# Performance work log

Hardware: AMD Instinct MI355X
Metric: run time of the kernel (lower is better)

## Reference

```python
import jax, jax.numpy as jnp
import numpy as np

N = 50000      # nodes
E = 200000     # edges
F_IN = 128     # input features
H = 1024       # hidden
C = 16         # classes
K = 3          # TAGConv hops
EPS = 1e-5


def setup_inputs() -> dict:
    key = jax.random.key(0)
    ks = jax.random.split(key, 12)
    s = 0.02
    x = jax.random.normal(ks[0], (N, F_IN), jnp.float32)
    edge_index = jax.random.randint(ks[1], (2, E), 0, N, dtype=jnp.int64)
    weight = jax.random.uniform(ks[2], (E,), jnp.float32)
    return {
        "x": x,
        "edge_index": edge_index,
        "weight": weight,
        "W1": jax.random.normal(ks[3], (K + 1, F_IN, H), jnp.float32) * s,
        "b1": jnp.zeros((H,), jnp.float32),
        "g1": jnp.ones((H,), jnp.float32),
        "be1": jnp.zeros((H,), jnp.float32),
        "a1": jnp.ones((H,), jnp.float32),
        "W2": jax.random.normal(ks[4], (K + 1, H, H), jnp.float32) * s,
        "b2": jnp.zeros((H,), jnp.float32),
        "g2": jnp.ones((H,), jnp.float32),
        "be2": jnp.zeros((H,), jnp.float32),
        "a2": jnp.ones((H,), jnp.float32),
        "W3": jax.random.normal(ks[5], (K + 1, H, C), jnp.float32) * s,
        "b3": jnp.zeros((C,), jnp.float32),
    }


def _edge_norm(weight, src, dst):
    # gcn_norm without self-loops: deg from edge weights at target nodes
    deg = jax.ops.segment_sum(weight, dst, num_segments=N)
    safe = jnp.where(deg > 0, deg, 1.0)
    dinv = jnp.where(deg > 0, jax.lax.rsqrt(safe), 0.0)
    norm_w = dinv[src] * weight * dinv[dst]
    cnt = jax.ops.segment_sum(jnp.ones((E,), weight.dtype), dst, num_segments=N)
    cnt_inv = jnp.where(cnt > 0, 1.0 / jnp.where(cnt > 0, cnt, 1.0), 0.0)
    return norm_w, cnt_inv


def _tagconv(x, W, b, src, dst, norm_w, cnt_inv):
    # out = sum_k lin_k(x_k), x_k = mean-aggr of norm_w * x_{k-1}[src] at dst
    out = x @ W[0]
    h = x
    for k in range(1, K + 1):
        msg = norm_w[:, None] * h[src]                       # [E, d]
        h = jax.ops.segment_sum(msg, dst, num_segments=N) * cnt_inv[:, None]
        out = out + h @ W[k]
    return out + b


def _graphnorm(x, g, be, a):
    # single graph: per-graph stats = global stats over nodes
    mean = jnp.mean(x, axis=0)
    out = x - a * mean
    var = jnp.mean(out * out, axis=0)
    return g * out / jnp.sqrt(var + EPS) + be


def reference(x, edge_index, weight, W1, b1, g1, be1, a1,
              W2, b2, g2, be2, a2, W3, b3):
    src, dst = edge_index[0], edge_index[1]
    norm_w, cnt_inv = _edge_norm(weight, src, dst)
    h = jax.nn.elu(_tagconv(x, W1, b1, src, dst, norm_w, cnt_inv))
    h = _graphnorm(h, g1, be1, a1)
    h = jax.nn.elu(_tagconv(h, W2, b2, src, dst, norm_w, cnt_inv))
    h = _graphnorm(h, g2, be2, a2)
    return _tagconv(h, W3, b3, src, dst, norm_w, cnt_inv)
```

## Files before the change

### kernel.cpp

```cpp
#include <hip/hip_runtime.h>
#include <hip/hip_bf16.h>
#include <math.h>

#define N_NODES 50000
#define N_EDGES 200000
#define FIN 128
#define HID 1024
#define NCLS 16
#define EPSN 1e-5f
#define NPAD 50048
#define MT 391
#define EPITCH 136

typedef __attribute__((ext_vector_type(8))) short short8;
typedef __attribute__((ext_vector_type(8))) unsigned short ushort8;
typedef __attribute__((ext_vector_type(4))) unsigned short u16x4;
typedef __attribute__((ext_vector_type(4))) float f32x4;

static __device__ __forceinline__ float bf2f(unsigned short u) {
  union { unsigned int i; float f; } v; v.i = ((unsigned int)u) << 16; return v.f;
}
static __device__ __forceinline__ unsigned short f2bf(float f) {
  __hip_bfloat16 h = __float2bfloat16(f);
  return *(unsigned short*)&h;
}

#define ASYNC16(gsrc, ldst)                                                   \
  __builtin_amdgcn_global_load_lds(                                           \
      (const __attribute__((address_space(1))) void*)(gsrc),                  \
      (__attribute__((address_space(3))) void*)(ldst), 16, 0, 0)


__global__ __launch_bounds__(256) void k_deg_cnt(const int* __restrict__ dst,
                                                 const float* __restrict__ w,
                                                 float* deg, int* cnt) {
  int e = blockIdx.x * 256 + threadIdx.x;
  if (e < N_EDGES) {
    int d = dst[e];
    atomicAdd(&deg[d], w[e]);
    atomicAdd(&cnt[d], 1);
  }
}

__global__ __launch_bounds__(256) void k_normw(const int* __restrict__ src,
                                               const int* __restrict__ dst,
                                               const float* __restrict__ w,
                                               const float* __restrict__ deg,
                                               float* __restrict__ normw) {
  int e = blockIdx.x * 256 + threadIdx.x;
  if (e < N_EDGES) {
    float ds = deg[src[e]], dd = deg[dst[e]];
    float a = ds > 0.f ? rsqrtf(ds) : 0.f;
    float b = dd > 0.f ? rsqrtf(dd) : 0.f;
    normw[e] = a * w[e] * b;
  }
}

__global__ __launch_bounds__(256) void k_cntinv(const int* __restrict__ cnt,
                                                float* __restrict__ cnt_inv) {
  int n = blockIdx.x * 256 + threadIdx.x;
  if (n < N_NODES) {
    int c = cnt[n];
    cnt_inv[n] = c > 0 ? 1.f / (float)c : 0.f;
  }
}

__global__ __launch_bounds__(1024) void k_scan_a(const int* __restrict__ cnt,
                                                 int* __restrict__ rowptr,
                                                 int* __restrict__ bsums) {
  __shared__ int sm[1024];
  int tid = threadIdx.x;
  int i = blockIdx.x * 1024 + tid;
  int v = (i < N_NODES) ? cnt[i] : 0;
  sm[tid] = v;
  __syncthreads();
  for (int off = 1; off < 1024; off <<= 1) {
    int t = (tid >= off) ? sm[tid - off] : 0;
    __syncthreads();
    sm[tid] += t;
    __syncthreads();
  }
  if (i < N_NODES) rowptr[i] = sm[tid] - v;
  if (tid == 1023) bsums[blockIdx.x] = sm[1023];
}

__global__ void k_scan_b(int* bsums, int nb) {
  if (threadIdx.x == 0 && blockIdx.x == 0) {
    int s = 0;
    for (int i = 0; i < nb; ++i) { int t = bsums[i]; bsums[i] = s; s += t; }
  }
}

__global__ __launch_bounds__(1024) void k_scan_c(int* __restrict__ rowptr,
                                                 const int* __restrict__ bsums) {
  int i = blockIdx.x * 1024 + threadIdx.x;
  if (i < N_NODES) rowptr[i] += bsums[blockIdx.x];
}

__global__ __launch_bounds__(256) void k_fill(const int* __restrict__ src,
                                              const int* __restrict__ dst,
                                              const float* __restrict__ normw,
                                              const int* __restrict__ rowptr,
                                              int* __restrict__ fill,
                                              int2* __restrict__ csr_ew) {
  int e = blockIdx.x * 256 + threadIdx.x;
  if (e < N_EDGES) {
    int d = dst[e];
    int pos = rowptr[d] + atomicAdd(&fill[d], 1);
    csr_ew[pos] = make_int2(src[e], __float_as_int(normw[e]));
  }
}


__global__ void k_transpose_bf16(const float* __restrict__ in,
                                 __hip_bfloat16* __restrict__ out, int K, int N) {
  __shared__ float tile[32][33];
  int kb = blockIdx.x * 32, nb = blockIdx.y * 32;
  int tx = threadIdx.x, ty = threadIdx.y;
  for (int i = ty; i < 32; i += 8) tile[i][tx] = in[(size_t)(kb + i) * N + nb + tx];
  __syncthreads();
  for (int i = ty; i < 32; i += 8)
    out[(size_t)(nb + i) * K + kb + tx] = __float2bfloat16(tile[tx][i]);
}

__global__ void k_transpose_scale_bf16(const float* __restrict__ in,
                                       __hip_bfloat16* __restrict__ out, int K, int N,
                                       const float* __restrict__ alpha) {
  __shared__ float tile[32][33];
  int kb = blockIdx.x * 32, nb = blockIdx.y * 32;
  int tx = threadIdx.x, ty = threadIdx.y;
  for (int i = ty; i < 32; i += 8) tile[i][tx] = in[(size_t)(kb + i) * N + nb + tx];
  __syncthreads();
  float sc = alpha[(kb + tx) & (HID - 1)];
  for (int i = ty; i < 32; i += 8)
    out[(size_t)(nb + i) * K + kb + tx] = __float2bfloat16(tile[tx][i] * sc);
}

__global__ __launch_bounds__(256) void k_ck(const float* __restrict__ W2,
                                            const float* __restrict__ beta,
                                            const float* __restrict__ b2,
                                            float* __restrict__ ck) {
  int k3 = blockIdx.x, tid = threadIdx.x;
  float acc[4] = {0.f, 0.f, 0.f, 0.f};
  const float* Wk = W2 + (size_t)k3 * HID * HID;
  for (int in = 0; in < HID; ++in) {
    float s = beta[in];
    const float* row = Wk + (size_t)in * HID;
#pragma unroll
    for (int j = 0; j < 4; ++j) acc[j] += s * row[tid + j * 256];
  }
#pragma unroll
  for (int j = 0; j < 4; ++j) {
    float v = acc[j];
    if (k3 == 0) v += b2[tid + j * 256];
    ck[k3 * HID + tid + j * 256] = v;
  }
}

__global__ __launch_bounds__(256) void k_packw3(const float* __restrict__ W3,
                                                __hip_bfloat16* __restrict__ W3T) {
  int idx = blockIdx.x * 256 + threadIdx.x;
  if (idx < 4 * 1024 * 16) {
    int k3 = idx >> 14, r = idx & 16383, k = r >> 4, j = r & 15;
    W3T[(size_t)(k3 * 16 + j) * 1024 + k] = __float2bfloat16(W3[idx]);
  }
}

__global__ __launch_bounds__(256) void k_x_to_bf16(const float* __restrict__ x,
                                                   unsigned short* __restrict__ xc) {
  int i = blockIdx.x * 256 + threadIdx.x;
  if (i < N_NODES * FIN / 4) {
    int n = i >> 5, c4 = i & 31;
    const float4 v = ((const float4*)x)[i];
    u16x4 o;
    o[0] = f2bf(v.x); o[1] = f2bf(v.y); o[2] = f2bf(v.z); o[3] = f2bf(v.w);
    *(u16x4*)&xc[(size_t)n * 512 + c4 * 4] = o;
  }
}


template <int W>
__global__ __launch_bounds__(256) void k_spmm_v(
    const unsigned short* __restrict__ src_t, int sp,
    unsigned short* __restrict__ dst_t, int dp,
    const int* __restrict__ rowptr, const int* __restrict__ cnt,
    const float* __restrict__ cnt_inv,
    const int2* __restrict__ csr_ew) {
  constexpr int G = W / 8;
  int gl = blockIdx.x * 256 + threadIdx.x;
  int node = gl / G;
  if (node >= N_NODES) return;
  int fl = (gl % G) * 8;
  int beg = rowptr[node], ne = cnt[node];
  float acc[8] = {0.f, 0.f, 0.f, 0.f, 0.f, 0.f, 0.f, 0.f};
  for (int i = 0; i < ne; ++i) {
    int2 e = csr_ew[beg + i];
    float wt = __int_as_float(e.y);
    ushort8 v = *(const ushort8*)&src_t[(size_t)e.x * sp + fl];
#pragma unroll
    for (int j = 0; j < 8; ++j) acc[j] += wt * bf2f(v[j]);
  }
  float ci = cnt_inv[node];
  ushort8 o;
#pragma unroll
  for (int j = 0; j < 8; ++j) o[j] = f2bf(acc[j] * ci);
  *(ushort8*)&dst_t[(size_t)node * dp + fl] = o;
}

__global__ __launch_bounds__(256) void k_spmm16(const float* __restrict__ src_t, int sp,
                                                const float* __restrict__ addend, int ap,
                                                const float* __restrict__ b3,
                                                float* __restrict__ out, int op,
                                                const int* __restrict__ rowptr,
                                                const int* __restrict__ cnt,
                                                const float* __restrict__ cnt_inv,
                                                const int2* __restrict__ csr_ew) {
  int idx = blockIdx.x * 256 + threadIdx.x;
  if (idx >= N_NODES * 16) return;
  int node = idx >> 4, f = idx & 15;
  int beg = rowptr[node], ne = cnt[node];
  float acc = 0.f;
  for (int i = 0; i < ne; ++i) {
    int2 e = csr_ew[beg + i];
    acc += __int_as_float(e.y) * src_t[(size_t)e.x * sp + f];
  }
  float r = acc * cnt_inv[node] + addend[(size_t)node * ap + f];
  if (b3) r += b3[f];
  out[(size_t)node * op + f] = r;
}


__global__ __launch_bounds__(256, 4) void k_gemm(
    const unsigned short* __restrict__ A, int lda,
    const unsigned short* __restrict__ BT, int ldb,
    const unsigned short* __restrict__ Cinit, int ldci,
    void* __restrict__ Cout, int ldc, int cbf16,
    int M, int Nout, int K,
    const float* __restrict__ bias, int do_elu) {
  __shared__ __align__(16) unsigned short smem[128 * EPITCH];
  int tid = threadIdx.x;
  int wave = tid >> 6, lane = tid & 63;
  int wm = wave >> 1, wn = wave & 1;
  int l15 = lane & 15, quad = lane >> 4;
  int im = blockIdx.y, in_ = blockIdx.x;

  f32x4 acc[4][4];
  if (Cinit) {
    {
      int r = tid >> 1, hf = tid & 1;
      const unsigned short* gsrc =
          &Cinit[(size_t)(im * 128 + r) * ldci + in_ * 128 + hf * 64];
#pragma unroll
      for (int v = 0; v < 8; ++v)
        *(ushort8*)&smem[r * EPITCH + hf * 64 + v * 8] = *(const ushort8*)&gsrc[v * 8];
    }
    __syncthreads();
#pragma unroll
    for (int i = 0; i < 4; ++i)
#pragma unroll
      for (int j = 0; j < 4; ++j)
#pragma unroll
        for (int reg = 0; reg < 4; ++reg)
          acc[i][j][reg] =
              bf2f(smem[(wm * 64 + i * 16 + quad * 4 + reg) * EPITCH + wn * 64 + j * 16 + l15]);
    __syncthreads();
  } else {
#pragma unroll
    for (int i = 0; i < 4; ++i)
#pragma unroll
      for (int j = 0; j < 4; ++j) acc[i][j] = (f32x4){0.f, 0.f, 0.f, 0.f};
  }

  int srow = tid >> 2;
  int sl = (tid & 3) ^ (srow & 3) ^ ((srow >> 2) & 3);
  const unsigned short* gA0 = &A[(size_t)(im * 128 + srow) * lda + sl * 8];
  const unsigned short* gA1 = &A[(size_t)(im * 128 + 64 + srow) * lda + sl * 8];
  const unsigned short* gB0 = &BT[(size_t)(in_ * 128 + srow) * ldb + sl * 8];
  const unsigned short* gB1 = &BT[(size_t)(in_ * 128 + 64 + srow) * ldb + sl * 8];
  unsigned short* ldsA = smem;
  unsigned short* ldsB = smem + 8192;
  int woff0 = (wave * 64) * 8;
  int woff1 = (256 + wave * 64) * 8;
  int rsl = (quad ^ (l15 & 3) ^ (l15 >> 2)) * 8;

  auto stage = [&](int k0, int p) {
    ASYNC16(gA0 + k0, &ldsA[p * 4096 + woff0]);
    ASYNC16(gA1 + k0, &ldsA[p * 4096 + woff1]);
    ASYNC16(gB0 + k0, &ldsB[p * 4096 + woff0]);
    ASYNC16(gB1 + k0, &ldsB[p * 4096 + woff1]);
  };
  auto compute = [&](int p) {
    short8 af[4], bf[4];
#pragma unroll
    for (int i = 0; i < 4; ++i)
      af[i] = *(const short8*)&ldsA[p * 4096 + (wm * 64 + i * 16 + l15) * 32 + rsl];
#pragma unroll
    for (int j = 0; j < 4; ++j)
      bf[j] = *(const short8*)&ldsB[p * 4096 + (wn * 64 + j * 16 + l15) * 32 + rsl];
#pragma unroll
    for (int i = 0; i < 4; ++i)
#pragma unroll
      for (int j = 0; j < 4; ++j)
        acc[i][j] = __builtin_amdgcn_mfma_f32_16x16x32_bf16(af[i], bf[j], acc[i][j], 0, 0, 0);
  };

  stage(0, 0);
  __syncthreads();
  int p = 0;
  for (int k0 = 32; k0 < K; k0 += 32) {
    stage(k0, p ^ 1);
    compute(p);
    __syncthreads();
    p ^= 1;
  }
  compute(p);
  __syncthreads();

  if (cbf16) {
#pragma unroll
    for (int i = 0; i < 4; ++i)
#pragma unroll
      for (int j = 0; j < 4; ++j) {
        int cg = in_ * 128 + wn * 64 + j * 16 + l15;
        float bv = bias ? bias[cg] : 0.f;
#pragma unroll
        for (int reg = 0; reg < 4; ++reg) {
          float v = acc[i][j][reg] + bv;
          if (do_elu) v = v > 0.f ? v : expm1f(v);
          smem[(wm * 64 + i * 16 + quad * 4 + reg) * EPITCH + wn * 64 + j * 16 + l15] = f2bf(v);
        }
      }
    __syncthreads();
    int r = tid >> 1, hf = tid & 1;
    unsigned short* gdst =
        (unsigned short*)Cout + (size_t)(im * 128 + r) * ldc + in_ * 128 + hf * 64;
#pragma unroll
    for (int v = 0; v < 8; ++v)
      *(ushort8*)&gdst[v * 8] = *(const ushort8*)&smem[r * EPITCH + hf * 64 + v * 8];
  } else {
#pragma unroll
    for (int i = 0; i < 4; ++i) {
      int r0 = im * 128 + wm * 64 + i * 16 + quad * 4;
#pragma unroll
      for (int j = 0; j < 4; ++j) {
        int c = in_ * 128 + wn * 64 + j * 16 + l15;
        if (c < Nout) {
#pragma unroll
          for (int reg = 0; reg < 4; ++reg) {
            int r = r0 + reg;
            if (r < M) {
              float v = acc[i][j][reg];
              if (bias) v += bias[c];
              if (do_elu) v = v > 0.f ? v : expm1f(v);
              ((float*)Cout)[(size_t)r * ldc + c] = v;
            }
          }
        }
      }
    }
  }
}


__global__ __launch_bounds__(512) void k_colstats(const unsigned short* __restrict__ h,
                                                  float* __restrict__ stats) {
  __shared__ float sm[4 * 2048];
  int tid = threadIdx.x;
  int f0 = (tid & 127) * 8;
  int q = tid >> 7;
  int r0 = blockIdx.y * 128 + q * 32;
  int r1 = r0 + 32; if (r1 > N_NODES) r1 = N_NODES;
  float s[8] = {0,0,0,0,0,0,0,0}, s2[8] = {0,0,0,0,0,0,0,0};
  for (int r = r0; r < r1; ++r) {
    ushort8 v = *(const ushort8*)&h[(size_t)r * HID + f0];
#pragma unroll
    for (int j = 0; j < 8; ++j) { float x = bf2f(v[j]); s[j] += x; s2[j] += x * x; }
  }
#pragma unroll
  for (int j = 0; j < 8; ++j) {
    sm[q * 2048 + f0 + j] = s[j];
    sm[q * 2048 + 1024 + f0 + j] = s2[j];
  }
  __syncthreads();
  for (int idx = tid; idx < 2048; idx += 512) {
    float v = sm[idx] + sm[2048 + idx] + sm[4096 + idx] + sm[6144 + idx];
    atomicAdd(&stats[idx], v);
  }
}

__global__ __launch_bounds__(256) void k_finalize(const float* __restrict__ g,
                                                  const float* __restrict__ be,
                                                  const float* __restrict__ a,
                                                  float* __restrict__ stats) {
  int f = blockIdx.x * 256 + threadIdx.x;
  if (f < HID) {
    float m = stats[f] / (float)N_NODES;
    float ex2 = stats[HID + f] / (float)N_NODES;
    float av = a[f];
    float var = ex2 - 2.f * av * m * m + av * av * m * m;
    float alpha = g[f] * rsqrtf(var + EPSN);
    stats[2 * HID + f] = alpha;
    stats[3 * HID + f] = be[f] - alpha * av * m;
  }
}

__global__ __launch_bounds__(256) void k_normalize(unsigned short* __restrict__ h,
                                                   const float* __restrict__ stats) {
  int i = blockIdx.x * 256 + threadIdx.x;
  if (i < N_NODES * HID / 8) {
    int f0 = (i * 8) & 1023;
    ushort8 v = *(ushort8*)&h[(size_t)i * 8];
#pragma unroll
    for (int j = 0; j < 8; ++j)
      v[j] = f2bf(stats[2 * HID + f0 + j] * bf2f(v[j]) + stats[3 * HID + f0 + j]);
    *(ushort8*)&h[(size_t)i * 8] = v;
  }
}


extern "C" void kernel_launch(void* const* d_in, const int* in_sizes, int n_in,
                              void* d_out, int out_size, void* d_ws, size_t ws_size,
                              hipStream_t stream) {
  const float* x   = (const float*)d_in[0];
  const int*   ei  = (const int*)d_in[1];
  const float* w   = (const float*)d_in[2];
  const float* W1  = (const float*)d_in[3];
  const float* b1  = (const float*)d_in[4];
  const float* g1  = (const float*)d_in[5];
  const float* be1 = (const float*)d_in[6];
  const float* a1  = (const float*)d_in[7];
  const float* W2  = (const float*)d_in[8];
  const float* b2  = (const float*)d_in[9];
  const float* g2  = (const float*)d_in[10];
  const float* be2 = (const float*)d_in[11];
  const float* a2  = (const float*)d_in[12];
  const float* W3  = (const float*)d_in[13];
  const float* b3  = (const float*)d_in[14];
  float* out = (float*)d_out;

  const int* srcI = ei;
  const int* dstI = ei + N_EDGES;

  char* base = (char*)d_ws;
  size_t off = 0;
  auto alloc = [&](size_t bytes) -> char* {
    char* p = base + off;
    off += (bytes + 255) & ~(size_t)255;
    return p;
  };

  float* deg      = (float*)alloc(N_NODES * 4);
  int*   cnt      = (int*)alloc(N_NODES * 4);
  float* cnt_inv  = (float*)alloc(N_NODES * 4);
  float* normw    = (float*)alloc(N_EDGES * 4);
  int*   rowptr   = (int*)alloc((N_NODES + 1) * 4);
  int*   fill     = (int*)alloc(N_NODES * 4);
  int*   bsums    = (int*)alloc(64 * 4);
  int2*  csr_ew   = (int2*)alloc((size_t)N_EDGES * 8);
  float* stats    = (float*)alloc(4 * HID * 4);
  float* ck       = (float*)alloc(4 * HID * 4);
  __hip_bfloat16* W1T = (__hip_bfloat16*)alloc((size_t)1024 * 512 * 2);
  __hip_bfloat16* W2T = (__hip_bfloat16*)alloc((size_t)1024 * 4096 * 2);
  __hip_bfloat16* W3T = (__hip_bfloat16*)alloc((size_t)128 * 1024 * 2);
  const size_t FT = (size_t)NPAD * HID * 2;
  unsigned short* T0 = (unsigned short*)alloc(FT);
  unsigned short* T1 = (unsigned short*)alloc(FT);
  size_t rem = (ws_size > off) ? (ws_size - off) : 0;
  bool full = rem >= FT + 1024;
  unsigned short *T2 = nullptr, *Q = nullptr, *R = nullptr;
  int wcols = 0;
  if (full) {
    T2 = (unsigned short*)alloc(FT);
  } else {
    wcols = 512;
    if (rem < 2 * (size_t)NPAD * 512 * 2 + 1024) wcols = 256;
    if (wcols == 256 && rem < 2 * (size_t)NPAD * 256 * 2 + 1024) wcols = 128;
    Q = (unsigned short*)alloc((size_t)NPAD * wcols * 2);
    R = (unsigned short*)alloc((size_t)NPAD * wcols * 2);
  }
  float* Z  = (float*)T0;
  float* t0 = (float*)((char*)T0 + (size_t)16 * 1024 * 1024);
  float* t1 = (float*)((char*)T0 + (size_t)24 * 1024 * 1024);
  (void)n_in; (void)in_sizes; (void)out_size;

  const int EB = (N_EDGES + 255) / 256;
  const int NB = (N_NODES + 255) / 256;

  (void)hipMemsetAsync(deg, 0, N_NODES * 4, stream);
  (void)hipMemsetAsync(cnt, 0, N_NODES * 4, stream);
  (void)hipMemsetAsync(fill, 0, N_NODES * 4, stream);
  k_deg_cnt<<<EB, 256, 0, stream>>>(dstI, w, deg, cnt);
  k_normw<<<EB, 256, 0, stream>>>(srcI, dstI, w, deg, normw);
  k_cntinv<<<NB, 256, 0, stream>>>(cnt, cnt_inv);
  k_scan_a<<<49, 1024, 0, stream>>>(cnt, rowptr, bsums);
  k_scan_b<<<1, 64, 0, stream>>>(bsums, 49);
  k_scan_c<<<49, 1024, 0, stream>>>(rowptr, bsums);
  k_fill<<<EB, 256, 0, stream>>>(srcI, dstI, normw, rowptr, fill, csr_ew);

  k_transpose_bf16<<<dim3(512 / 32, 1024 / 32), dim3(32, 8), 0, stream>>>(W1, W1T, 512, 1024);
  k_packw3<<<(65536 + 255) / 256, 256, 0, stream>>>(W3, W3T);

  const unsigned short* W2Tu = (const unsigned short*)W2T;

  k_x_to_bf16<<<(N_NODES * FIN / 4 + 255) / 256, 256, 0, stream>>>(x, T1);
  {
    int blocks = (N_NODES * 16 + 255) / 256;
    for (int k = 1; k <= 3; ++k)
      k_spmm_v<128><<<blocks, 256, 0, stream>>>(
          T1 + (k - 1) * FIN, 512, T1 + k * FIN, 512,
          rowptr, cnt, cnt_inv, csr_ew);
  }
  k_gemm<<<dim3(8, MT), 256, 0, stream>>>(
      T1, 512, (const unsigned short*)W1T, 512,
      nullptr, 0, T0, HID, 1, N_NODES, HID, 512, b1, 1);
  (void)hipMemsetAsync(stats, 0, 2 * HID * 4, stream);
  k_colstats<<<dim3(1, MT), 512, 0, stream>>>(T0, stats);
  k_finalize<<<4, 256, 0, stream>>>(g1, be1, a1, stats);
  k_transpose_scale_bf16<<<dim3(4096 / 32, 1024 / 32), dim3(32, 8), 0, stream>>>(
      W2, W2T, 4096, 1024, stats + 2 * HID);
  k_ck<<<4, 256, 0, stream>>>(W2, stats + 3 * HID, b2, ck);

  if (full) {
    const int SPB = (N_NODES * 128 + 255) / 256;
    k_gemm<<<dim3(8, MT), 256, 0, stream>>>(
        T0, 1024, W2Tu + 3 * 1024, 4096,
        nullptr, 0, T1, 1024, 1, N_NODES, 1024, 1024, ck + 3 * 1024, 0);
    k_spmm_v<1024><<<SPB, 256, 0, stream>>>(T1, 1024, T2, 1024,
                                            rowptr, cnt, cnt_inv, csr_ew);
    k_gemm<<<dim3(8, MT), 256, 0, stream>>>(
        T0, 1024, W2Tu + 2 * 1024, 4096,
        T2, 1024, T1, 1024, 1, N_NODES, 1024, 1024, ck + 2 * 1024, 0);
    k_spmm_v<1024><<<SPB, 256, 0, stream>>>(T1, 1024, T2, 1024,
                                            rowptr, cnt, cnt_inv, csr_ew);
    k_gemm<<<dim3(8, MT), 256, 0, stream>>>(
        T0, 1024, W2Tu + 1 * 1024, 4096,
        T2, 1024, T1, 1024, 1, N_NODES, 1024, 1024, ck + 1 * 1024, 0);
    k_spmm_v<1024><<<SPB, 256, 0, stream>>>(T1, 1024, T2, 1024,
                                            rowptr, cnt, cnt_inv, csr_ew);
    k_gemm<<<dim3(8, MT), 256, 0, stream>>>(
        T0, 1024, W2Tu + 0 * 1024, 4096,
        T2, 1024, T1, 1024, 1, N_NODES, 1024, 1024, ck + 0 * 1024, 1);
  } else {
    auto spmm_w = [&](const unsigned short* s, unsigned short* d) {
      int blocks = (N_NODES * (wcols / 8) + 255) / 256;
      if (wcols == 512)
        k_spmm_v<512><<<blocks, 256, 0, stream>>>(s, wcols, d, wcols,
            rowptr, cnt, cnt_inv, csr_ew);
      else if (wcols == 256)
        k_spmm_v<256><<<blocks, 256, 0, stream>>>(s, wcols, d, wcols,
            rowptr, cnt, cnt_inv, csr_ew);
      else
        k_spmm_v<128><<<blocks, 256, 0, stream>>>(s, wcols, d, wcols,
            rowptr, cnt, cnt_inv, csr_ew);
    };
    for (int c = 0; c < HID; c += wcols) {
      const unsigned short* Wb = W2Tu + (size_t)c * 4096;
      k_gemm<<<dim3(wcols / 128, MT), 256, 0, stream>>>(
          T0, 1024, Wb + 3 * 1024, 4096,
          nullptr, 0, Q, wcols, 1, N_NODES, wcols, 1024, ck + 3 * 1024 + c, 0);
      spmm_w(Q, R);
      k_gemm<<<dim3(wcols / 128, MT), 256, 0, stream>>>(
          T0, 1024, Wb + 2 * 1024, 4096,
          R, wcols, Q, wcols, 1, N_NODES, wcols, 1024, ck + 2 * 1024 + c, 0);
      spmm_w(Q, R);
      k_gemm<<<dim3(wcols / 128, MT), 256, 0, stream>>>(
          T0, 1024, Wb + 1 * 1024, 4096,
          R, wcols, Q, wcols, 1, N_NODES, wcols, 1024, ck + 1 * 1024 + c, 0);
      spmm_w(Q, R);
      k_gemm<<<dim3(wcols / 128, MT), 256, 0, stream>>>(
          T0, 1024, Wb + 0 * 1024, 4096,
          R, wcols, T1 + c, 1024, 1, N_NODES, wcols, 1024, ck + 0 * 1024 + c, 1);
    }
  }
  (void)hipMemsetAsync(stats, 0, 2 * HID * 4, stream);
  k_colstats<<<dim3(1, MT), 512, 0, stream>>>(T1, stats);
  k_finalize<<<4, 256, 0, stream>>>(g2, be2, a2, stats);
  k_normalize<<<(N_NODES * HID / 8) / 256, 256, 0, stream>>>(T1, stats);

  k_gemm<<<dim3(1, MT), 256, 0, stream>>>(
      T1, 1024, (const unsigned short*)W3T, 1024,
      nullptr, 0, Z, 64, 0, N_NODES, 64, 1024, nullptr, 0);
  const int SB = (N_NODES * 16 + 255) / 256;
  k_spmm16<<<SB, 256, 0, stream>>>(Z + 48, 64, Z + 32, 64, nullptr, t0, 16,
                                   rowptr, cnt, cnt_inv, csr_ew);
  k_spmm16<<<SB, 256, 0, stream>>>(t0, 16, Z + 16, 64, nullptr, t1, 16,
                                   rowptr, cnt, cnt_inv, csr_ew);
  k_spmm16<<<SB, 256, 0, stream>>>(t1, 16, Z + 0, 64, b3, out, 16,
                                   rowptr, cnt, cnt_inv, csr_ew);
}
```

Before: 1.978 ms.

## Fuse graphnorm column stats into GEMM epilogue and fold second norm into W3

Column sum and sum-of-squares are now accumulated in the bf16 GEMM epilogue from shared memory with atomics, which removes the separate colstats passes over the 50000x1024 activations. The second graphnorm's per-column affine is folded into W3 (scaled by alpha) and a bias term ck3, so the full normalize pass over T1 is gone. The LDS pitch changes to 132 with 8-byte accesses to cut bank conflicts, and the SpMM gather loop is unrolled by two edges. The cost is a serial per-column loop over 128 rows inside each GEMM block plus global atomics, and stats are taken from bf16-rounded outputs.

```diff
diff --git a/kernel.cpp b/kernel.cpp
--- a/kernel.cpp
+++ b/kernel.cpp
@@ -10,7 +10,7 @@
 #define EPSN 1e-5f
 #define NPAD 50048
 #define MT 391
-#define EPITCH 136
+#define EPITCH 132
 
 typedef __attribute__((ext_vector_type(8))) short short8;
 typedef __attribute__((ext_vector_type(8))) unsigned short ushort8;
@@ -157,12 +157,24 @@
   }
 }
 
+__global__ __launch_bounds__(64) void k_ck3(const float* __restrict__ W3,
+                                            const float* __restrict__ beta,
+                                            float* __restrict__ ck3) {
+  int t = threadIdx.x;
+  int k = t >> 4, j = t & 15;
+  float acc = 0.f;
+  for (int in = 0; in < HID; ++in)
+    acc += beta[in] * W3[((size_t)k * HID + in) * 16 + j];
+  ck3[t] = acc;
+}
+
 __global__ __launch_bounds__(256) void k_packw3(const float* __restrict__ W3,
-                                                __hip_bfloat16* __restrict__ W3T) {
+                                                __hip_bfloat16* __restrict__ W3T,
+                                                const float* __restrict__ alpha) {
   int idx = blockIdx.x * 256 + threadIdx.x;
   if (idx < 4 * 1024 * 16) {
     int k3 = idx >> 14, r = idx & 16383, k = r >> 4, j = r & 15;
-    W3T[(size_t)(k3 * 16 + j) * 1024 + k] = __float2bfloat16(W3[idx]);
+    W3T[(size_t)(k3 * 16 + j) * 1024 + k] = __float2bfloat16(W3[idx] * alpha[k]);
   }
 }
 
@@ -191,14 +203,23 @@
   int node = gl / G;
   if (node >= N_NODES) return;
   int fl = (gl % G) * 8;
-  int beg = rowptr[node], ne = cnt[node];
+  int beg = rowptr[node], end = beg + cnt[node];
   float acc[8] = {0.f, 0.f, 0.f, 0.f, 0.f, 0.f, 0.f, 0.f};
-  for (int i = 0; i < ne; ++i) {
-    int2 e = csr_ew[beg + i];
-    float wt = __int_as_float(e.y);
-    ushort8 v = *(const ushort8*)&src_t[(size_t)e.x * sp + fl];
-#pragma unroll
-    for (int j = 0; j < 8; ++j) acc[j] += wt * bf2f(v[j]);
+  int i = beg;
+  for (; i + 1 < end; i += 2) {
+    int2 e0 = csr_ew[i], e1 = csr_ew[i + 1];
+    float w0 = __int_as_float(e0.y), w1 = __int_as_float(e1.y);
+    ushort8 v0 = *(const ushort8*)&src_t[(size_t)e0.x * sp + fl];
+    ushort8 v1 = *(const ushort8*)&src_t[(size_t)e1.x * sp + fl];
+#pragma unroll
+    for (int j = 0; j < 8; ++j) acc[j] += w0 * bf2f(v0[j]) + w1 * bf2f(v1[j]);
+  }
+  if (i < end) {
+    int2 e0 = csr_ew[i];
+    float w0 = __int_as_float(e0.y);
+    ushort8 v0 = *(const ushort8*)&src_t[(size_t)e0.x * sp + fl];
+#pragma unroll
+    for (int j = 0; j < 8; ++j) acc[j] += w0 * bf2f(v0[j]);
   }
   float ci = cnt_inv[node];
   ushort8 o;
@@ -236,7 +257,8 @@
     const unsigned short* __restrict__ Cinit, int ldci,
     void* __restrict__ Cout, int ldc, int cbf16,
     int M, int Nout, int K,
-    const float* __restrict__ bias, int do_elu) {
+    const float* __restrict__ bias, int do_elu,
+    float* __restrict__ stats_out, int stats_off) {
   __shared__ __align__(16) unsigned short smem[128 * EPITCH];
   int tid = threadIdx.x;
   int wave = tid >> 6, lane = tid & 63;
@@ -251,8 +273,14 @@
       const unsigned short* gsrc =
           &Cinit[(size_t)(im * 128 + r) * ldci + in_ * 128 + hf * 64];
 #pragma unroll
-      for (int v = 0; v < 8; ++v)
-        *(ushort8*)&smem[r * EPITCH + hf * 64 + v * 8] = *(const ushort8*)&gsrc[v * 8];
+      for (int v = 0; v < 8; ++v) {
+        ushort8 t8 = *(const ushort8*)&gsrc[v * 8];
+        u16x4 lo, hi;
+        lo[0] = t8[0]; lo[1] = t8[1]; lo[2] = t8[2]; lo[3] = t8[3];
+        hi[0] = t8[4]; hi[1] = t8[5]; hi[2] = t8[6]; hi[3] = t8[7];
+        *(u16x4*)&smem[r * EPITCH + hf * 64 + v * 8] = lo;
+        *(u16x4*)&smem[r * EPITCH + hf * 64 + v * 8 + 4] = hi;
+      }
     }
     __syncthreads();
 #pragma unroll
@@ -335,8 +363,24 @@
     unsigned short* gdst =
         (unsigned short*)Cout + (size_t)(im * 128 + r) * ldc + in_ * 128 + hf * 64;
 #pragma unroll
-    for (int v = 0; v < 8; ++v)
-      *(ushort8*)&gdst[v * 8] = *(const ushort8*)&smem[r * EPITCH + hf * 64 + v * 8];
+    for (int v = 0; v < 8; ++v) {
+      u16x4 lo = *(const u16x4*)&smem[r * EPITCH + hf * 64 + v * 8];
+      u16x4 hi = *(const u16x4*)&smem[r * EPITCH + hf * 64 + v * 8 + 4];
+      ushort8 o;
+      o[0] = lo[0]; o[1] = lo[1]; o[2] = lo[2]; o[3] = lo[3];
+      o[4] = hi[0]; o[5] = hi[1]; o[6] = hi[2]; o[7] = hi[3];
+      *(ushort8*)&gdst[v * 8] = o;
+    }
+    if (stats_out && tid < 128) {
+      int rmax = M - im * 128; if (rmax > 128) rmax = 128;
+      float s = 0.f, s2 = 0.f;
+      for (int r2 = 0; r2 < rmax; ++r2) {
+        float v = bf2f(smem[r2 * EPITCH + tid]);
+        s += v; s2 += v * v;
+      }
+      atomicAdd(&stats_out[stats_off + in_ * 128 + tid], s);
+      atomicAdd(&stats_out[HID + stats_off + in_ * 128 + tid], s2);
+    }
   } else {
 #pragma unroll
     for (int i = 0; i < 4; ++i) {
@@ -361,32 +405,6 @@
   }
 }
 
-
-__global__ __launch_bounds__(512) void k_colstats(const unsigned short* __restrict__ h,
-                                                  float* __restrict__ stats) {
-  __shared__ float sm[4 * 2048];
-  int tid = threadIdx.x;
-  int f0 = (tid & 127) * 8;
-  int q = tid >> 7;
-  int r0 = blockIdx.y * 128 + q * 32;
-  int r1 = r0 + 32; if (r1 > N_NODES) r1 = N_NODES;
-  float s[8] = {0,0,0,0,0,0,0,0}, s2[8] = {0,0,0,0,0,0,0,0};
-  for (int r = r0; r < r1; ++r) {
-    ushort8 v = *(const ushort8*)&h[(size_t)r * HID + f0];
-#pragma unroll
-    for (int j = 0; j < 8; ++j) { float x = bf2f(v[j]); s[j] += x; s2[j] += x * x; }
-  }
-#pragma unroll
-  for (int j = 0; j < 8; ++j) {
-    sm[q * 2048 + f0 + j] = s[j];
-    sm[q * 2048 + 1024 + f0 + j] = s2[j];
-  }
-  __syncthreads();
-  for (int idx = tid; idx < 2048; idx += 512) {
-    float v = sm[idx] + sm[2048 + idx] + sm[4096 + idx] + sm[6144 + idx];
-    atomicAdd(&stats[idx], v);
-  }
-}
 
 __global__ __launch_bounds__(256) void k_finalize(const float* __restrict__ g,
                                                   const float* __restrict__ be,
@@ -401,19 +419,6 @@
     float alpha = g[f] * rsqrtf(var + EPSN);
     stats[2 * HID + f] = alpha;
     stats[3 * HID + f] = be[f] - alpha * av * m;
-  }
-}
-
-__global__ __launch_bounds__(256) void k_normalize(unsigned short* __restrict__ h,
-                                                   const float* __restrict__ stats) {
-  int i = blockIdx.x * 256 + threadIdx.x;
-  if (i < N_NODES * HID / 8) {
-    int f0 = (i * 8) & 1023;
-    ushort8 v = *(ushort8*)&h[(size_t)i * 8];
-#pragma unroll
-    for (int j = 0; j < 8; ++j)
-      v[j] = f2bf(stats[2 * HID + f0 + j] * bf2f(v[j]) + stats[3 * HID + f0 + j]);
-    *(ushort8*)&h[(size_t)i * 8] = v;
   }
 }
 
@@ -459,6 +464,7 @@
   int2*  csr_ew   = (int2*)alloc((size_t)N_EDGES * 8);
   float* stats    = (float*)alloc(4 * HID * 4);
   float* ck       = (float*)alloc(4 * HID * 4);
+  float* ck3      = (float*)alloc(64 * 4);
   __hip_bfloat16* W1T = (__hip_bfloat16*)alloc((size_t)1024 * 512 * 2);
   __hip_bfloat16* W2T = (__hip_bfloat16*)alloc((size_t)1024 * 4096 * 2);
   __hip_bfloat16* W3T = (__hip_bfloat16*)alloc((size_t)128 * 1024 * 2);
@@ -498,7 +504,6 @@
   k_fill<<<EB, 256, 0, stream>>>(srcI, dstI, normw, rowptr, fill, csr_ew);
 
   k_transpose_bf16<<<dim3(512 / 32, 1024 / 32), dim3(32, 8), 0, stream>>>(W1, W1T, 512, 1024);
-  k_packw3<<<(65536 + 255) / 256, 256, 0, stream>>>(W3, W3T);
 
   const unsigned short* W2Tu = (const unsigned short*)W2T;
 
@@ -510,11 +515,10 @@
           T1 + (k - 1) * FIN, 512, T1 + k * FIN, 512,
           rowptr, cnt, cnt_inv, csr_ew);
   }
+  (void)hipMemsetAsync(stats, 0, 2 * HID * 4, stream);
   k_gemm<<<dim3(8, MT), 256, 0, stream>>>(
       T1, 512, (const unsigned short*)W1T, 512,
-      nullptr, 0, T0, HID, 1, N_NODES, HID, 512, b1, 1);
-  (void)hipMemsetAsync(stats, 0, 2 * HID * 4, stream);
-  k_colstats<<<dim3(1, MT), 512, 0, stream>>>(T0, stats);
+      nullptr, 0, T0, HID, 1, N_NODES, HID, 512, b1, 1, stats, 0);
   k_finalize<<<4, 256, 0, stream>>>(g1, be1, a1, stats);
   k_transpose_scale_bf16<<<dim3(4096 / 32, 1024 / 32), dim3(32, 8), 0, stream>>>(
       W2, W2T, 4096, 1024, stats + 2 * HID);
@@ -524,22 +528,23 @@
     const int SPB = (N_NODES * 128 + 255) / 256;
     k_gemm<<<dim3(8, MT), 256, 0, stream>>>(
         T0, 1024, W2Tu + 3 * 1024, 4096,
-        nullptr, 0, T1, 1024, 1, N_NODES, 1024, 1024, ck + 3 * 1024, 0);
+        nullptr, 0, T1, 1024, 1, N_NODES, 1024, 1024, ck + 3 * 1024, 0, nullptr, 0);
     k_spmm_v<1024><<<SPB, 256, 0, stream>>>(T1, 1024, T2, 1024,
                                             rowptr, cnt, cnt_inv, csr_ew);
     k_gemm<<<dim3(8, MT), 256, 0, stream>>>(
         T0, 1024, W2Tu + 2 * 1024, 4096,
-        T2, 1024, T1, 1024, 1, N_NODES, 1024, 1024, ck + 2 * 1024, 0);
+        T2, 1024, T1, 1024, 1, N_NODES, 1024, 1024, ck + 2 * 1024, 0, nullptr, 0);
     k_spmm_v<1024><<<SPB, 256, 0, stream>>>(T1, 1024, T2, 1024,
                                             rowptr, cnt, cnt_inv, csr_ew);
     k_gemm<<<dim3(8, MT), 256, 0, stream>>>(
         T0, 1024, W2Tu + 1 * 1024, 4096,
-        T2, 1024, T1, 1024, 1, N_NODES, 1024, 1024, ck + 1 * 1024, 0);
+        T2, 1024, T1, 1024, 1, N_NODES, 1024, 1024, ck + 1 * 1024, 0, nullptr, 0);
     k_spmm_v<1024><<<SPB, 256, 0, stream>>>(T1, 1024, T2, 1024,
                                             rowptr, cnt, cnt_inv, csr_ew);
+    (void)hipMemsetAsync(stats, 0, 2 * HID * 4, stream);
     k_gemm<<<dim3(8, MT), 256, 0, stream>>>(
         T0, 1024, W2Tu + 0 * 1024, 4096,
-        T2, 1024, T1, 1024, 1, N_NODES, 1024, 1024, ck + 0 * 1024, 1);
+        T2, 1024, T1, 1024, 1, N_NODES, 1024, 1024, ck + 0 * 1024, 1, stats, 0);
   } else {
     auto spmm_w = [&](const unsigned short* s, unsigned short* d) {
       int blocks = (N_NODES * (wcols / 8) + 255) / 256;
@@ -553,33 +558,33 @@
         k_spmm_v<128><<<blocks, 256, 0, stream>>>(s, wcols, d, wcols,
             rowptr, cnt, cnt_inv, csr_ew);
     };
+    (void)hipMemsetAsync(stats, 0, 2 * HID * 4, stream);
     for (int c = 0; c < HID; c += wcols) {
       const unsigned short* Wb = W2Tu + (size_t)c * 4096;
       k_gemm<<<dim3(wcols / 128, MT), 256, 0, stream>>>(
           T0, 1024, Wb + 3 * 1024, 4096,
-          nullptr, 0, Q, wcols, 1, N_NODES, wcols, 1024, ck + 3 * 1024 + c, 0);
+          nullptr, 0, Q, wcols, 1, N_NODES, wcols, 1024, ck + 3 * 1024 + c, 0, nullptr, 0);
       spmm_w(Q, R);
       k_gemm<<<dim3(wcols / 128, MT), 256, 0, stream>>>(
           T0, 1024, Wb + 2 * 1024, 4096,
-          R, wcols, Q, wcols, 1, N_NODES, wcols, 1024, ck + 2 * 1024 + c, 0);
+          R, wcols, Q, wcols, 1, N_NODES, wcols, 1024, ck + 2 * 1024 + c, 0, nullptr, 0);
       spmm_w(Q, R);
       k_gemm<<<dim3(wcols / 128, MT), 256, 0, stream>>>(
           T0, 1024, Wb + 1 * 1024, 4096,
-          R, wcols, Q, wcols, 1, N_NODES, wcols, 1024, ck + 1 * 1024 + c, 0);
+          R, wcols, Q, wcols, 1, N_NODES, wcols, 1024, ck + 1 * 1024 + c, 0, nullptr, 0);
       spmm_w(Q, R);
       k_gemm<<<dim3(wcols / 128, MT), 256, 0, stream>>>(
           T0, 1024, Wb + 0 * 1024, 4096,
-          R, wcols, T1 + c, 1024, 1, N_NODES, wcols, 1024, ck + 0 * 1024 + c, 1);
+          R, wcols, T1 + c, 1024, 1, N_NODES, wcols, 1024, ck + 0 * 1024 + c, 1, stats, c);
     }
   }
-  (void)hipMemsetAsync(stats, 0, 2 * HID * 4, stream);
-  k_colstats<<<dim3(1, MT), 512, 0, stream>>>(T1, stats);
   k_finalize<<<4, 256, 0, stream>>>(g2, be2, a2, stats);
-  k_normalize<<<(N_NODES * HID / 8) / 256, 256, 0, stream>>>(T1, stats);
+  k_packw3<<<(65536 + 255) / 256, 256, 0, stream>>>(W3, W3T, stats + 2 * HID);
+  k_ck3<<<1, 64, 0, stream>>>(W3, stats + 3 * HID, ck3);
 
   k_gemm<<<dim3(1, MT), 256, 0, stream>>>(
       T1, 1024, (const unsigned short*)W3T, 1024,
-      nullptr, 0, Z, 64, 0, N_NODES, 64, 1024, nullptr, 0);
+      nullptr, 0, Z, 64, 0, N_NODES, 64, 1024, ck3, 0, nullptr, 0);
   const int SB = (N_NODES * 16 + 255) / 256;
   k_spmm16<<<SB, 256, 0, stream>>>(Z + 48, 64, Z + 32, 64, nullptr, t0, 16,
                                    rowptr, cnt, cnt_inv, csr_ew);
```

Result: faster. 1.919 ms (-3.0%).

## Fold second GraphNorm into W3 weights and bias, parallelize ck, unroll SpMM

Applied to the files above, without the earlier changes.

Removes the k_normalize pass over the 50000x1024 hidden tensor. The per-feature scale is folded into the packed W3 weights and the shift into a per-output bias (ck3) added in the final GEMM epilogue. Also splits the ck bias computation across 16 input chunks with atomic accumulation instead of 4 serial blocks, and unrolls the SpMM edge loop by two to get more loads in flight. Folding the normalization into the weights changes where bf16 rounding happens, and the bias path now depends on the GEMM epilogue correctly handling a bias when the last flag is 0.

```diff
diff --git a/kernel.cpp b/kernel.cpp
--- a/kernel.cpp
+++ b/kernel.cpp
@@ -136,14 +136,17 @@
     out[(size_t)(nb + i) * K + kb + tx] = __float2bfloat16(tile[tx][i] * sc);
 }
 
-__global__ __launch_bounds__(256) void k_ck(const float* __restrict__ W2,
-                                            const float* __restrict__ beta,
-                                            const float* __restrict__ b2,
-                                            float* __restrict__ ck) {
-  int k3 = blockIdx.x, tid = threadIdx.x;
+__global__ __launch_bounds__(256) void k_ck_part(const float* __restrict__ W2,
+                                                 const float* __restrict__ beta,
+                                                 const float* __restrict__ b2,
+                                                 float* __restrict__ ck) {
+  int k3 = blockIdx.x;
+  int ch = blockIdx.y;
+  int tid = threadIdx.x;
   float acc[4] = {0.f, 0.f, 0.f, 0.f};
   const float* Wk = W2 + (size_t)k3 * HID * HID;
-  for (int in = 0; in < HID; ++in) {
+  int i0 = ch * 64;
+  for (int in = i0; in < i0 + 64; ++in) {
     float s = beta[in];
     const float* row = Wk + (size_t)in * HID;
 #pragma unroll
@@ -152,17 +155,29 @@
 #pragma unroll
   for (int j = 0; j < 4; ++j) {
     float v = acc[j];
-    if (k3 == 0) v += b2[tid + j * 256];
-    ck[k3 * HID + tid + j * 256] = v;
-  }
+    if (k3 == 0 && ch == 0) v += b2[tid + j * 256];
+    atomicAdd(&ck[k3 * HID + tid + j * 256], v);
+  }
+}
+
+__global__ __launch_bounds__(64) void k_ck3(const float* __restrict__ W3,
+                                            const float* __restrict__ beta,
+                                            float* __restrict__ ck3) {
+  int t = threadIdx.x;
+  int k = t >> 4, j = t & 15;
+  float acc = 0.f;
+  for (int in = 0; in < HID; ++in)
+    acc += beta[in] * W3[((size_t)k * HID + in) * 16 + j];
+  ck3[t] = acc;
 }
 
 __global__ __launch_bounds__(256) void k_packw3(const float* __restrict__ W3,
-                                                __hip_bfloat16* __restrict__ W3T) {
+                                                __hip_bfloat16* __restrict__ W3T,
+                                                const float* __restrict__ alpha) {
   int idx = blockIdx.x * 256 + threadIdx.x;
   if (idx < 4 * 1024 * 16) {
     int k3 = idx >> 14, r = idx & 16383, k = r >> 4, j = r & 15;
-    W3T[(size_t)(k3 * 16 + j) * 1024 + k] = __float2bfloat16(W3[idx]);
+    W3T[(size_t)(k3 * 16 + j) * 1024 + k] = __float2bfloat16(W3[idx] * alpha[k]);
   }
 }
 
@@ -191,14 +206,23 @@
   int node = gl / G;
   if (node >= N_NODES) return;
   int fl = (gl % G) * 8;
-  int beg = rowptr[node], ne = cnt[node];
+  int beg = rowptr[node], end = beg + cnt[node];
   float acc[8] = {0.f, 0.f, 0.f, 0.f, 0.f, 0.f, 0.f, 0.f};
-  for (int i = 0; i < ne; ++i) {
-    int2 e = csr_ew[beg + i];
-    float wt = __int_as_float(e.y);
-    ushort8 v = *(const ushort8*)&src_t[(size_t)e.x * sp + fl];
-#pragma unroll
-    for (int j = 0; j < 8; ++j) acc[j] += wt * bf2f(v[j]);
+  int i = beg;
+  for (; i + 1 < end; i += 2) {
+    int2 e0 = csr_ew[i], e1 = csr_ew[i + 1];
+    float w0 = __int_as_float(e0.y), w1 = __int_as_float(e1.y);
+    ushort8 v0 = *(const ushort8*)&src_t[(size_t)e0.x * sp + fl];
+    ushort8 v1 = *(const ushort8*)&src_t[(size_t)e1.x * sp + fl];
+#pragma unroll
+    for (int j = 0; j < 8; ++j) acc[j] += w0 * bf2f(v0[j]) + w1 * bf2f(v1[j]);
+  }
+  if (i < end) {
+    int2 e0 = csr_ew[i];
+    float w0 = __int_as_float(e0.y);
+    ushort8 v0 = *(const ushort8*)&src_t[(size_t)e0.x * sp + fl];
+#pragma unroll
+    for (int j = 0; j < 8; ++j) acc[j] += w0 * bf2f(v0[j]);
   }
   float ci = cnt_inv[node];
   ushort8 o;
@@ -401,19 +425,6 @@
     float alpha = g[f] * rsqrtf(var + EPSN);
     stats[2 * HID + f] = alpha;
     stats[3 * HID + f] = be[f] - alpha * av * m;
-  }
-}
-
-__global__ __launch_bounds__(256) void k_normalize(unsigned short* __restrict__ h,
-                                                   const float* __restrict__ stats) {
-  int i = blockIdx.x * 256 + threadIdx.x;
-  if (i < N_NODES * HID / 8) {
-    int f0 = (i * 8) & 1023;
-    ushort8 v = *(ushort8*)&h[(size_t)i * 8];
-#pragma unroll
-    for (int j = 0; j < 8; ++j)
-      v[j] = f2bf(stats[2 * HID + f0 + j] * bf2f(v[j]) + stats[3 * HID + f0 + j]);
-    *(ushort8*)&h[(size_t)i * 8] = v;
   }
 }
 
@@ -459,6 +470,7 @@
   int2*  csr_ew   = (int2*)alloc((size_t)N_EDGES * 8);
   float* stats    = (float*)alloc(4 * HID * 4);
   float* ck       = (float*)alloc(4 * HID * 4);
+  float* ck3      = (float*)alloc(64 * 4);
   __hip_bfloat16* W1T = (__hip_bfloat16*)alloc((size_t)1024 * 512 * 2);
   __hip_bfloat16* W2T = (__hip_bfloat16*)alloc((size_t)1024 * 4096 * 2);
   __hip_bfloat16* W3T = (__hip_bfloat16*)alloc((size_t)128 * 1024 * 2);
@@ -498,7 +510,6 @@
   k_fill<<<EB, 256, 0, stream>>>(srcI, dstI, normw, rowptr, fill, csr_ew);
 
   k_transpose_bf16<<<dim3(512 / 32, 1024 / 32), dim3(32, 8), 0, stream>>>(W1, W1T, 512, 1024);
-  k_packw3<<<(65536 + 255) / 256, 256, 0, stream>>>(W3, W3T);
 
   const unsigned short* W2Tu = (const unsigned short*)W2T;
 
@@ -518,7 +529,8 @@
   k_finalize<<<4, 256, 0, stream>>>(g1, be1, a1, stats);
   k_transpose_scale_bf16<<<dim3(4096 / 32, 1024 / 32), dim3(32, 8), 0, stream>>>(
       W2, W2T, 4096, 1024, stats + 2 * HID);
-  k_ck<<<4, 256, 0, stream>>>(W2, stats + 3 * HID, b2, ck);
+  (void)hipMemsetAsync(ck, 0, 4 * HID * 4, stream);
+  k_ck_part<<<dim3(4, 16), 256, 0, stream>>>(W2, stats + 3 * HID, b2, ck);
 
   if (full) {
     const int SPB = (N_NODES * 128 + 255) / 256;
@@ -575,11 +587,12 @@
   (void)hipMemsetAsync(stats, 0, 2 * HID * 4, stream);
   k_colstats<<<dim3(1, MT), 512, 0, stream>>>(T1, stats);
   k_finalize<<<4, 256, 0, stream>>>(g2, be2, a2, stats);
-  k_normalize<<<(N_NODES * HID / 8) / 256, 256, 0, stream>>>(T1, stats);
+  k_packw3<<<(65536 + 255) / 256, 256, 0, stream>>>(W3, W3T, stats + 2 * HID);
+  k_ck3<<<1, 64, 0, stream>>>(W3, stats + 3 * HID, ck3);
 
   k_gemm<<<dim3(1, MT), 256, 0, stream>>>(
       T1, 1024, (const unsigned short*)W3T, 1024,
-      nullptr, 0, Z, 64, 0, N_NODES, 64, 1024, nullptr, 0);
+      nullptr, 0, Z, 64, 0, N_NODES, 64, 1024, ck3, 0);
   const int SB = (N_NODES * 16 + 255) / 256;
   k_spmm16<<<SB, 256, 0, stream>>>(Z + 48, 64, Z + 32, 64, nullptr, t0, 16,
                                    rowptr, cnt, cnt_inv, csr_ew);
```

New measurement: 1.835 ms. -7.2%, faster.
